# Kernel tuning notes

Hardware: AMD Instinct MI355X
Metric: run time of the kernel (lower is better)

The kernel has to match this reference:

```python
import jax, jax.numpy as jnp
import numpy as np

B, N, D, H, DK, DV, E = 32, 512, 128, 8, 16, 16, 128
MLP_H = 16


def _uniform(key, shape, fan):
    s = 1.0 / np.sqrt(fan)
    return jax.random.uniform(key, shape, jnp.float32, -s, s)


def setup_inputs() -> dict:
    key = jax.random.key(0)
    ks = jax.random.split(key, 13)
    q = jax.random.normal(ks[0], (B, N, D), jnp.float32)
    mask = jax.random.randint(ks[1], (B, N, N), 0, 2) > 0  # True = attention not allowed
    edge_matrix = jax.random.normal(ks[2], (B, N, N), jnp.float32)
    # per-head projection weights (init: uniform(-1/sqrt(last_dim), ...))
    W_query = _uniform(ks[3], (H, D, DK), DK)
    W_key = _uniform(ks[4], (H, D, DK), DK)
    W_val = _uniform(ks[5], (H, D, DV), DV)
    W_out = _uniform(ks[6], (H, DV, E), E)
    # edge MLP: 1 -> 16 -> 16 -> n_heads, ReLU between layers
    mlp_W1 = _uniform(ks[7], (1, MLP_H), 1)
    mlp_b1 = _uniform(ks[8], (MLP_H,), 1)
    mlp_W2 = _uniform(ks[9], (MLP_H, MLP_H), MLP_H)
    mlp_b2 = _uniform(ks[10], (MLP_H,), MLP_H)
    mlp_W3 = _uniform(ks[11], (MLP_H, H), MLP_H)
    mlp_b3 = _uniform(ks[12], (H,), MLP_H)
    return dict(q=q, mask=mask, edge_matrix=edge_matrix,
                W_query=W_query, W_key=W_key, W_val=W_val, W_out=W_out,
                mlp_W1=mlp_W1, mlp_b1=mlp_b1, mlp_W2=mlp_W2, mlp_b2=mlp_b2,
                mlp_W3=mlp_W3, mlp_b3=mlp_b3)


def reference(q, mask, edge_matrix, W_query, W_key, W_val, W_out,
              mlp_W1, mlp_b1, mlp_W2, mlp_b2, mlp_W3, mlp_b3):
    dk = W_query.shape[-1]
    norm = 1.0 / np.sqrt(dk)
    # per-head projections: [H,B,N,dk]
    Q = jnp.einsum('bni,hid->hbnd', q, W_query)
    K = jnp.einsum('bni,hid->hbnd', q, W_key)
    V = jnp.einsum('bni,hid->hbnd', q, W_val)
    # scaled QK^T: [H,B,N,N]
    comp = norm * jnp.einsum('hbqd,hbkd->hbqk', Q, K)
    # edge-bias MLP on each scalar edge weight: [B,N,N,1] -> [B,N,N,H]
    e = edge_matrix[..., None]
    h1 = jax.nn.relu(e @ mlp_W1 + mlp_b1)
    h2 = jax.nn.relu(h1 @ mlp_W2 + mlp_b2)
    bias = h2 @ mlp_W3 + mlp_b3
    comp = comp + jnp.transpose(bias, (3, 0, 1, 2))
    # masked softmax (mask True = disallowed)
    m = mask[None]  # broadcast over heads
    comp = jnp.where(m, -jnp.inf, comp)
    attn = jax.nn.softmax(comp, axis=-1)
    attn = jnp.where(m, 0.0, attn)
    heads = jnp.einsum('hbqk,hbkd->hbqd', attn, V)  # [H,B,N,dv]
    out = jnp.einsum('hbqd,hde->bqe', heads, W_out)  # [B,N,E]
    return out
```

## Files before the change

kernel.cpp:

```cpp
#include <hip/hip_runtime.h>
#include <hip/hip_bf16.h>
#include <float.h>

#define Bc 32
#define Nc 512
#define Dc 128
#define Hc 8
#define DKc 16
#define Ec 128
#define LOG2E 1.44269504088896340736f
#define SCLAMP 80.0f

typedef __attribute__((ext_vector_type(4))) short s16x4;
typedef __attribute__((ext_vector_type(8))) short s16x8;
typedef __attribute__((ext_vector_type(4))) float f32x4;

union BFU { __hip_bfloat16 b; short s; };
static __device__ inline short f2bf(float f) { BFU u; u.b = __float2bfloat16(f); return u.s; }
static __device__ inline s16x4 pack4(float a, float b, float c, float d) {
  s16x4 r; r[0] = f2bf(a); r[1] = f2bf(b); r[2] = f2bf(c); r[3] = f2bf(d); return r;
}

#if __has_builtin(__builtin_amdgcn_exp2f)
#define EXP2F(x) __builtin_amdgcn_exp2f(x)
#else
#define EXP2F(x) exp2f(x)
#endif

static __device__ inline f32x4 mfma16(s16x4 a, s16x4 b, f32x4 c) {
#if __has_builtin(__builtin_amdgcn_mfma_f32_16x16x16bf16_1k)
  return __builtin_amdgcn_mfma_f32_16x16x16bf16_1k(a, b, c, 0, 0, 0);
#else
  int lane = threadIdx.x & 63;
  int g = lane >> 4, base = lane & 15;
  int src0 = (base + 32 * g) & 63;
  int src1 = (base + 32 * g + 16) & 63;
  int ax = ((int*)&a)[0], ay = ((int*)&a)[1];
  int bx = ((int*)&b)[0], by = ((int*)&b)[1];
  int A0 = __shfl(ax, src0), A1 = __shfl(ay, src0);
  int A2 = __shfl(ax, src1), A3 = __shfl(ay, src1);
  int B0 = __shfl(bx, src0), B1 = __shfl(by, src0);
  int B2 = __shfl(bx, src1), B3 = __shfl(by, src1);
  if (g >= 2) { A0 = A1 = A2 = A3 = 0; B0 = B1 = B2 = B3 = 0; }
  s16x8 A8, B8;
  ((int*)&A8)[0] = A0; ((int*)&A8)[1] = A1; ((int*)&A8)[2] = A2; ((int*)&A8)[3] = A3;
  ((int*)&B8)[0] = B0; ((int*)&B8)[1] = B1; ((int*)&B8)[2] = B2; ((int*)&B8)[3] = B3;
  return __builtin_amdgcn_mfma_f32_16x16x32_bf16(A8, B8, c, 0, 0, 0);
#endif
}

__global__ __launch_bounds__(256) void prep_all(
    const float* __restrict__ Wq, const float* __restrict__ Wk, const float* __restrict__ Wv,
    const float* __restrict__ Wo,
    const unsigned char* __restrict__ m, int* __restrict__ flag,
    const float* __restrict__ mW1, const float* __restrict__ mb1,
    const float* __restrict__ mW2, const float* __restrict__ mb2,
    const float* __restrict__ mW3, const float* __restrict__ mb3,
    short* __restrict__ Wt, short* __restrict__ Wob, int* __restrict__ tabI)
{
  int blk = blockIdx.x;
  int t = threadIdx.x;

  if (blk == 256) {
    __shared__ int red[4];
    int any = 0;
    for (int u = t; u < 16384; u += 256)
      if ((u & 3) != 0 && m[u] != 0) any = 1;
    unsigned long long bal = __ballot(any != 0);
    if ((t & 63) == 0) red[t >> 6] = (bal != 0ULL) ? 1 : 0;
    __syncthreads();
    if (t == 0) *flag = red[0] | red[1] | red[2] | red[3];
    return;
  }

  if (blk >= 257) {
    __shared__ float wl[440];
    for (int u = t; u < 440; u += 256) {
      float v;
      if (u < 16) v = mW1[u];
      else if (u < 32)  v = mb1[u - 16];
      else if (u < 288) v = mW2[u - 32];
      else if (u < 304) v = mb2[u - 288];
      else if (u < 432) v = mW3[u - 304];
      else v = mb3[u - 432];
      wl[u] = v;
    }
    __syncthreads();
    int c = (blk - 257) * 256 + t;
    float mm = fmaf((float)c, 0.015625f, -7.9921875f);

    float pre[16];
    #pragma unroll
    for (int u = 0; u < 16; ++u) pre[u] = fmaf(mm, wl[u], wl[16 + u]);
    float a2[16], v2[16];
    #pragma unroll
    for (int v = 0; v < 16; ++v) { a2[v] = 0.f; v2[v] = wl[288 + v]; }
    #pragma unroll
    for (int u = 0; u < 16; ++u) {
      bool act = pre[u] > 0.f;
      float w1 = act ? wl[u] : 0.f;
      float pp = act ? pre[u] : 0.f;
      #pragma unroll
      for (int v = 0; v < 16; ++v) {
        float w2 = wl[32 + u * 16 + v];
        a2[v] = fmaf(w1, w2, a2[v]);
        v2[v] = fmaf(pp, w2, v2[v]);
      }
    }
    float ah[8], fh[8];
    #pragma unroll
    for (int h = 0; h < 8; ++h) { ah[h] = 0.f; fh[h] = wl[432 + h]; }
    #pragma unroll
    for (int v = 0; v < 16; ++v) {
      bool act = v2[v] > 0.f;
      float av = act ? a2[v] : 0.f;
      float vv = act ? v2[v] : 0.f;
      #pragma unroll
      for (int h = 0; h < 8; ++h) {
        float w3 = wl[304 + v * 8 + h];
        ah[h] = fmaf(av, w3, ah[h]);
        fh[h] = fmaf(vv, w3, fh[h]);
      }
    }
    #pragma unroll
    for (int h = 0; h < 8; ++h) {
      int ab = (int)(unsigned short)(f2bf(ah[h] * LOG2E));
      int fb = ((int)f2bf(fh[h] * LOG2E)) << 16;
      tabI[h * 1024 + c] = fb | ab;
    }
    return;
  }

  int o = blk * 256 + t;
  if (o < 49152) {
    int mat = o >> 14, r = o & 16383;
    int hk = r >> 7, d = r & 127;
    const float* src = (mat == 0) ? Wq : ((mat == 1) ? Wk : Wv);
    Wt[o] = f2bf(src[(hk >> 4) * 2048 + d * 16 + (hk & 15)]);
  } else {
    int o2 = o - 49152;
    int et = o2 >> 11, s = (o2 >> 8) & 7, lane = (o2 >> 2) & 63, i = o2 & 3;
    Wob[o2] = f2bf(Wo[(s * 16 + (lane >> 4) * 4 + i) * 128 + et * 16 + (lane & 15)]);
  }
}

__global__ __launch_bounds__(256, 4) void qkv4(
    const float* __restrict__ q, const short* __restrict__ Wt,
    short* __restrict__ Qb, short* __restrict__ Kb, short* __restrict__ Vt)
{
  __shared__ short qs[16][136];
  int blk = blockIdx.x;
  int b = blk >> 5;
  int rt = (blk & 31) << 4;
  int t = threadIdx.x;
  int wid = t >> 6, lane = t & 63;
  int lq = lane & 15, lg = lane >> 4;

  #pragma unroll
  for (int it = 0; it < 2; ++it) {
    int u = t + it * 256;
    int row = u >> 5, c4 = (u & 31) << 2;
    float4 v = *(const float4*)&q[((((b << 9) + rt + row) << 7)) + c4];
    *(s16x4*)&qs[row][c4] = pack4(v.x, v.y, v.z, v.w);
  }
  __syncthreads();

  s16x4 af[8];
  #pragma unroll
  for (int ks = 0; ks < 8; ++ks)
    af[ks] = *(const s16x4*)&qs[lq][ks * 16 + lg * 4];

  #pragma unroll 1
  for (int pj = 0; pj < 3; ++pj) {
    const short* Wm = Wt + pj * 16384;
    #pragma unroll
    for (int c2 = 0; c2 < 2; ++c2) {
      int ct = wid * 2 + c2;
      f32x4 acc = (f32x4)0.f;
      #pragma unroll
      for (int ks = 0; ks < 8; ++ks) {
        s16x4 bf = *(const s16x4*)&Wm[(ct * 16 + lq) * 128 + ks * 16 + lg * 4];
        acc = mfma16(af[ks], bf, acc);
      }
      if (pj == 0) {
        s16x4 pk = pack4(acc[0] * (0.25f * LOG2E), acc[1] * (0.25f * LOG2E),
                         acc[2] * (0.25f * LOG2E), acc[3] * (0.25f * LOG2E));
        #pragma unroll
        for (int r = 0; r < 4; ++r)
          Qb[(ct << 18) + (b << 13) + ((rt + lg * 4 + r) << 4) + lq] = pk[r];
      } else if (pj == 1) {
        s16x4 pk = pack4(acc[0], acc[1], acc[2], acc[3]);
        #pragma unroll
        for (int r = 0; r < 4; ++r)
          Kb[(ct << 18) + (b << 13) + ((rt + lg * 4 + r) << 4) + lq] = pk[r];
      } else {
        s16x4 pk = pack4(acc[0], acc[1], acc[2], acc[3]);
        *(s16x4*)&Vt[(ct << 18) + (((b << 4) + lq) << 9) + rt + lg * 4] = pk;
      }
    }
  }
}

__global__ __launch_bounds__(512, 4) void attn11(
    const float* __restrict__ edge, const unsigned char* __restrict__ maskB,
    const int* __restrict__ flag,
    const short* __restrict__ Qb, const short* __restrict__ Kb, const short* __restrict__ Vt,
    const short* __restrict__ Wob,
    const int* __restrict__ tabI,
    float* __restrict__ out)
{
  __shared__ __align__(16) char smem[36864];

  int t = threadIdx.x;
  int wid = t >> 6, lane = t & 63;
  int lq = lane & 15, lg = lane >> 4;
  int b = blockIdx.x >> 5;
  int qt = (blockIdx.x & 31) << 4;
  int mflag = *flag;

  int* tabL = (int*)smem;
  s16x4* obfL = (s16x4*)smem;
  float* psL = (float*)(smem + 32768);

  for (int u = t; u < 2048; u += 512)
    ((int4*)smem)[u] = ((const int4*)tabI)[u];

  const short* Kl = Kb + (b << 13) + (lq << 4) + (lg << 2);
  const short* Vl = Vt + (((b << 4) + lq) << 9) + (lg << 2);
  const short* Ql = Qb + (b << 13) + ((qt + lq) << 4) + (lg << 2);
  unsigned mbase = (((b << 9) + qt + lq) << 9) + (lg << 2);

  s16x4 qf[8];
  #pragma unroll
  for (int h = 0; h < 8; ++h) qf[h] = *(const s16x4*)(Ql + (h << 18));

  f32x4 oacc[8];
  float psum[8];
  #pragma unroll
  for (int h = 0; h < 8; ++h) { oacc[h] = (f32x4)0.f; psum[h] = 0.f; }

  int jb = wid << 4;
  float4 ev = *(const float4*)&edge[mbase + jb];
  int4 mkv;
  if (mflag) {
    uchar4 u = *(const uchar4*)&maskB[mbase + jb];
    mkv.x = u.x; mkv.y = u.y; mkv.z = u.z; mkv.w = u.w;
  } else {
    mkv = *(const int4*)&((const int*)maskB)[mbase + jb];
  }

  __syncthreads();

#define DOHEAD(h) { \
    int c0 = tabL[((h) << 10) + ix0], c1 = tabL[((h) << 10) + ix1]; \
    int c2 = tabL[((h) << 10) + ix2], c3 = tabL[((h) << 10) + ix3]; \
    s16x4 kf = *(const s16x4*)(Kl + ((h) << 18) + (jb << 4)); \
    f32x4 sc; \
    sc[0] = fmaf(__int_as_float(c0 << 16), em0, __int_as_float(c0 & 0xffff0000)); \
    sc[1] = fmaf(__int_as_float(c1 << 16), em1, __int_as_float(c1 & 0xffff0000)); \
    sc[2] = fmaf(__int_as_float(c2 << 16), em2, __int_as_float(c2 & 0xffff0000)); \
    sc[3] = fmaf(__int_as_float(c3 << 16), em3, __int_as_float(c3 & 0xffff0000)); \
    sc = mfma16(kf, qf[h], sc); \
    s16x4 vf = *(const s16x4*)(Vl + ((h) << 18) + jb); \
    float p0 = mkv.x ? 0.f : EXP2F(fminf(sc[0], SCLAMP)); \
    float p1 = mkv.y ? 0.f : EXP2F(fminf(sc[1], SCLAMP)); \
    float p2 = mkv.z ? 0.f : EXP2F(fminf(sc[2], SCLAMP)); \
    float p3 = mkv.w ? 0.f : EXP2F(fminf(sc[3], SCLAMP)); \
    psum[h] += (p0 + p1) + (p2 + p3); \
    s16x4 pf = pack4(p0, p1, p2, p3); \
    oacc[h] = mfma16(vf, pf, oacc[h]); }

  #pragma unroll 1
  for (int cc = 0; cc < 4; ++cc) {
    jb = ((cc << 3) | wid) << 4;

    float fx0 = fminf(fmaxf(fmaf(ev.x, 64.f, 512.f), 0.f), 1023.f);
    float fx1 = fminf(fmaxf(fmaf(ev.y, 64.f, 512.f), 0.f), 1023.f);
    float fx2 = fminf(fmaxf(fmaf(ev.z, 64.f, 512.f), 0.f), 1023.f);
    float fx3 = fminf(fmaxf(fmaf(ev.w, 64.f, 512.f), 0.f), 1023.f);
    int ix0 = (int)fx0, ix1 = (int)fx1, ix2 = (int)fx2, ix3 = (int)fx3;
    float em0 = ev.x - fmaf((float)ix0, 0.015625f, -7.9921875f);
    float em1 = ev.y - fmaf((float)ix1, 0.015625f, -7.9921875f);
    float em2 = ev.z - fmaf((float)ix2, 0.015625f, -7.9921875f);
    float em3 = ev.w - fmaf((float)ix3, 0.015625f, -7.9921875f);

    float4 evn; int4 mkn;
    if (cc < 3) {
      int jbn = (((cc + 1) << 3) | wid) << 4;
      evn = *(const float4*)&edge[mbase + jbn];
      if (mflag) {
        uchar4 u = *(const uchar4*)&maskB[mbase + jbn];
        mkn.x = u.x; mkn.y = u.y; mkn.z = u.z; mkn.w = u.w;
      } else {
        mkn = *(const int4*)&((const int*)maskB)[mbase + jbn];
      }
    } else { evn = ev; mkn = mkv; }

    DOHEAD(0) DOHEAD(1) DOHEAD(2) DOHEAD(3)
    DOHEAD(4) DOHEAD(5) DOHEAD(6) DOHEAD(7)

    ev = evn; mkv = mkn;
  }
#undef DOHEAD

  #pragma unroll
  for (int h = 0; h < 8; ++h) {
    float s = psum[h];
    s += __shfl_xor(s, 16);
    s += __shfl_xor(s, 32);
    psum[h] = s;
  }
  if (lg == 0) {
    #pragma unroll
    for (int h = 0; h < 8; ++h) psL[(wid << 7) + (h << 4) + lq] = psum[h];
  }
  __syncthreads();

  #pragma unroll
  for (int h = 0; h < 8; ++h) {
    float tot = 0.f;
    #pragma unroll
    for (int w2 = 0; w2 < 8; ++w2) tot += psL[(w2 << 7) + (h << 4) + lq];
    float inv = (tot > 0.f) ? 1.f / tot : 0.f;
    obfL[((wid << 3) + h << 6) + lane] =
        pack4(oacc[h][0] * inv, oacc[h][1] * inv, oacc[h][2] * inv, oacc[h][3] * inv);
  }
  __syncthreads();

  {
    f32x4 d2a = (f32x4)0.f;
    #pragma unroll
    for (int s = 0; s < 8; ++s) {
      f32x4 fa = (f32x4)0.f;
      #pragma unroll
      for (int w2 = 0; w2 < 8; ++w2) {
        union { s16x4 v; int i[2]; } bb;
        bb.v = obfL[((w2 << 3) + s << 6) + lane];
        fa[0] += __int_as_float(bb.i[0] << 16);
        fa[1] += __int_as_float(bb.i[0] & 0xffff0000);
        fa[2] += __int_as_float(bb.i[1] << 16);
        fa[3] += __int_as_float(bb.i[1] & 0xffff0000);
      }
      s16x4 ob = pack4(fa[0], fa[1], fa[2], fa[3]);
      s16x4 wo = *(const s16x4*)&Wob[(((wid << 3) + s) << 8) + (lane << 2)];
      d2a = mfma16(wo, ob, d2a);
    }
    *(float4*)&out[((((b << 9) + qt + lq) << 7)) + (wid << 4) + (lg << 2)] =
        *(float4*)&d2a;
  }
}

extern "C" void kernel_launch(void* const* d_in, const int* in_sizes, int n_in,
                              void* d_out, int out_size, void* d_ws, size_t ws_size,
                              hipStream_t stream)
{
  const float* q    = (const float*)d_in[0];
  const unsigned char* mask = (const unsigned char*)d_in[1];
  const float* edge = (const float*)d_in[2];
  const float* Wq   = (const float*)d_in[3];
  const float* Wk   = (const float*)d_in[4];
  const float* Wv   = (const float*)d_in[5];
  const float* Wo   = (const float*)d_in[6];
  const float* mW1  = (const float*)d_in[7];
  const float* mb1  = (const float*)d_in[8];
  const float* mW2  = (const float*)d_in[9];
  const float* mb2  = (const float*)d_in[10];
  const float* mW3  = (const float*)d_in[11];
  const float* mb3  = (const float*)d_in[12];
  float* out = (float*)d_out;

  size_t per = (size_t)Hc * Bc * Nc * DKc;
  short* Wt  = (short*)d_ws;
  short* Wob = Wt + 49152;
  short* Qb  = Wob + 16384;
  short* Kb  = Qb + per;
  short* Vt  = Kb + per;
  int* tabI  = (int*)(Vt + per);
  int* flag  = tabI + 8192;

  prep_all<<<dim3(261), dim3(256), 0, stream>>>(Wq, Wk, Wv, Wo, mask, flag,
      mW1, mb1, mW2, mb2, mW3, mb3, Wt, Wob, tabI);
  qkv4<<<dim3(Bc * 32), dim3(256), 0, stream>>>(q, Wt, Qb, Kb, Vt);
  attn11<<<dim3(Bc * 32), dim3(512), 0, stream>>>(edge, mask, flag, Qb, Kb, Vt, Wob,
      tabI, out);
}
```

Before: 123.7 us.

## Assign one head per wave in attention kernel, removing cross-wave reduction

Each wave now processes a single head over all keys instead of all heads over a 1/8 key slice. This drops the LDS-based cross-wave reduction of softmax sums and output accumulators, shrinks per-thread state from eight accumulators to one, and lets each wave read its own head's slice of the edge-bias table. In exchange, every wave re-reads the full edge and mask rows for its queries, relying on cache to absorb the eightfold redundant loads.

New measurement: 146.9 us. 1.19x slower.

```diff
diff --git a/kernel.cpp b/kernel.cpp
--- a/kernel.cpp
+++ b/kernel.cpp
@@ -201,7 +201,7 @@
   }
 }
 
-__global__ __launch_bounds__(512, 4) void attn11(
+__global__ __launch_bounds__(512, 4) void attn12(
     const float* __restrict__ edge, const unsigned char* __restrict__ maskB,
     const int* __restrict__ flag,
     const short* __restrict__ Qb, const short* __restrict__ Kb, const short* __restrict__ Vt,
@@ -209,7 +209,7 @@
     const int* __restrict__ tabI,
     float* __restrict__ out)
 {
-  __shared__ __align__(16) char smem[36864];
+  __shared__ __align__(16) char smem[32768];
 
   int t = threadIdx.x;
   int wid = t >> 6, lane = t & 63;
@@ -218,61 +218,34 @@
   int qt = (blockIdx.x & 31) << 4;
   int mflag = *flag;
 
-  int* tabL = (int*)smem;
-  s16x4* obfL = (s16x4*)smem;
-  float* psL = (float*)(smem + 32768);
+  int* tabH = (int*)smem + (wid << 10);
 
   for (int u = t; u < 2048; u += 512)
     ((int4*)smem)[u] = ((const int4*)tabI)[u];
 
-  const short* Kl = Kb + (b << 13) + (lq << 4) + (lg << 2);
-  const short* Vl = Vt + (((b << 4) + lq) << 9) + (lg << 2);
-  const short* Ql = Qb + (b << 13) + ((qt + lq) << 4) + (lg << 2);
+  const short* Kl = Kb + (wid << 18) + (b << 13) + (lq << 4) + (lg << 2);
+  const short* Vl = Vt + (wid << 18) + (((b << 4) + lq) << 9) + (lg << 2);
+  const short* Ql = Qb + (wid << 18) + (b << 13) + ((qt + lq) << 4) + (lg << 2);
   unsigned mbase = (((b << 9) + qt + lq) << 9) + (lg << 2);
 
-  s16x4 qf[8];
-  #pragma unroll
-  for (int h = 0; h < 8; ++h) qf[h] = *(const s16x4*)(Ql + (h << 18));
-
-  f32x4 oacc[8];
-  float psum[8];
-  #pragma unroll
-  for (int h = 0; h < 8; ++h) { oacc[h] = (f32x4)0.f; psum[h] = 0.f; }
-
-  int jb = wid << 4;
-  float4 ev = *(const float4*)&edge[mbase + jb];
+  s16x4 qf = *(const s16x4*)Ql;
+  f32x4 oacc = (f32x4)0.f;
+  float psum = 0.f;
+
+  float4 ev = *(const float4*)&edge[mbase];
   int4 mkv;
   if (mflag) {
-    uchar4 u = *(const uchar4*)&maskB[mbase + jb];
+    uchar4 u = *(const uchar4*)&maskB[mbase];
     mkv.x = u.x; mkv.y = u.y; mkv.z = u.z; mkv.w = u.w;
   } else {
-    mkv = *(const int4*)&((const int*)maskB)[mbase + jb];
+    mkv = *(const int4*)&((const int*)maskB)[mbase];
   }
 
   __syncthreads();
 
-#define DOHEAD(h) { \
-    int c0 = tabL[((h) << 10) + ix0], c1 = tabL[((h) << 10) + ix1]; \
-    int c2 = tabL[((h) << 10) + ix2], c3 = tabL[((h) << 10) + ix3]; \
-    s16x4 kf = *(const s16x4*)(Kl + ((h) << 18) + (jb << 4)); \
-    f32x4 sc; \
-    sc[0] = fmaf(__int_as_float(c0 << 16), em0, __int_as_float(c0 & 0xffff0000)); \
-    sc[1] = fmaf(__int_as_float(c1 << 16), em1, __int_as_float(c1 & 0xffff0000)); \
-    sc[2] = fmaf(__int_as_float(c2 << 16), em2, __int_as_float(c2 & 0xffff0000)); \
-    sc[3] = fmaf(__int_as_float(c3 << 16), em3, __int_as_float(c3 & 0xffff0000)); \
-    sc = mfma16(kf, qf[h], sc); \
-    s16x4 vf = *(const s16x4*)(Vl + ((h) << 18) + jb); \
-    float p0 = mkv.x ? 0.f : EXP2F(fminf(sc[0], SCLAMP)); \
-    float p1 = mkv.y ? 0.f : EXP2F(fminf(sc[1], SCLAMP)); \
-    float p2 = mkv.z ? 0.f : EXP2F(fminf(sc[2], SCLAMP)); \
-    float p3 = mkv.w ? 0.f : EXP2F(fminf(sc[3], SCLAMP)); \
-    psum[h] += (p0 + p1) + (p2 + p3); \
-    s16x4 pf = pack4(p0, p1, p2, p3); \
-    oacc[h] = mfma16(vf, pf, oacc[h]); }
-
-  #pragma unroll 1
-  for (int cc = 0; cc < 4; ++cc) {
-    jb = ((cc << 3) | wid) << 4;
+  #pragma unroll 2
+  for (int cc = 0; cc < 32; ++cc) {
+    int jb = cc << 4;
 
     float fx0 = fminf(fmaxf(fmaf(ev.x, 64.f, 512.f), 0.f), 1023.f);
     float fx1 = fminf(fmaxf(fmaf(ev.y, 64.f, 512.f), 0.f), 1023.f);
@@ -284,9 +257,13 @@
     float em2 = ev.z - fmaf((float)ix2, 0.015625f, -7.9921875f);
     float em3 = ev.w - fmaf((float)ix3, 0.015625f, -7.9921875f);
 
+    int c0 = tabH[ix0], c1 = tabH[ix1], c2 = tabH[ix2], c3 = tabH[ix3];
+    s16x4 kf = *(const s16x4*)(Kl + (jb << 4));
+    s16x4 vf = *(const s16x4*)(Vl + jb);
+
     float4 evn; int4 mkn;
-    if (cc < 3) {
-      int jbn = (((cc + 1) << 3) | wid) << 4;
+    if (cc < 31) {
+      int jbn = (cc + 1) << 4;
       evn = *(const float4*)&edge[mbase + jbn];
       if (mflag) {
         uchar4 u = *(const uchar4*)&maskB[mbase + jbn];
@@ -296,53 +273,38 @@
       }
     } else { evn = ev; mkn = mkv; }
 
-    DOHEAD(0) DOHEAD(1) DOHEAD(2) DOHEAD(3)
-    DOHEAD(4) DOHEAD(5) DOHEAD(6) DOHEAD(7)
+    f32x4 sc;
+    sc[0] = fmaf(__int_as_float(c0 << 16), em0, __int_as_float(c0 & 0xffff0000));
+    sc[1] = fmaf(__int_as_float(c1 << 16), em1, __int_as_float(c1 & 0xffff0000));
+    sc[2] = fmaf(__int_as_float(c2 << 16), em2, __int_as_float(c2 & 0xffff0000));
+    sc[3] = fmaf(__int_as_float(c3 << 16), em3, __int_as_float(c3 & 0xffff0000));
+    sc = mfma16(kf, qf, sc);
+    float p0 = mkv.x ? 0.f : EXP2F(fminf(sc[0], SCLAMP));
+    float p1 = mkv.y ? 0.f : EXP2F(fminf(sc[1], SCLAMP));
+    float p2 = mkv.z ? 0.f : EXP2F(fminf(sc[2], SCLAMP));
+    float p3 = mkv.w ? 0.f : EXP2F(fminf(sc[3], SCLAMP));
+    psum += (p0 + p1) + (p2 + p3);
+    s16x4 pf = pack4(p0, p1, p2, p3);
+    oacc = mfma16(vf, pf, oacc);
 
     ev = evn; mkv = mkn;
   }
-#undef DOHEAD
-
-  #pragma unroll
-  for (int h = 0; h < 8; ++h) {
-    float s = psum[h];
-    s += __shfl_xor(s, 16);
-    s += __shfl_xor(s, 32);
-    psum[h] = s;
-  }
-  if (lg == 0) {
-    #pragma unroll
-    for (int h = 0; h < 8; ++h) psL[(wid << 7) + (h << 4) + lq] = psum[h];
-  }
-  __syncthreads();
-
-  #pragma unroll
-  for (int h = 0; h < 8; ++h) {
-    float tot = 0.f;
-    #pragma unroll
-    for (int w2 = 0; w2 < 8; ++w2) tot += psL[(w2 << 7) + (h << 4) + lq];
-    float inv = (tot > 0.f) ? 1.f / tot : 0.f;
-    obfL[((wid << 3) + h << 6) + lane] =
-        pack4(oacc[h][0] * inv, oacc[h][1] * inv, oacc[h][2] * inv, oacc[h][3] * inv);
-  }
+
+  float s = psum;
+  s += __shfl_xor(s, 16);
+  s += __shfl_xor(s, 32);
+  float inv = (s > 0.f) ? 1.f / s : 0.f;
+
+  *(s16x4*)(smem + (wid << 12) + lane * 8) =
+      pack4(oacc[0] * inv, oacc[1] * inv, oacc[2] * inv, oacc[3] * inv);
   __syncthreads();
 
   {
     f32x4 d2a = (f32x4)0.f;
     #pragma unroll
-    for (int s = 0; s < 8; ++s) {
-      f32x4 fa = (f32x4)0.f;
-      #pragma unroll
-      for (int w2 = 0; w2 < 8; ++w2) {
-        union { s16x4 v; int i[2]; } bb;
-        bb.v = obfL[((w2 << 3) + s << 6) + lane];
-        fa[0] += __int_as_float(bb.i[0] << 16);
-        fa[1] += __int_as_float(bb.i[0] & 0xffff0000);
-        fa[2] += __int_as_float(bb.i[1] << 16);
-        fa[3] += __int_as_float(bb.i[1] & 0xffff0000);
-      }
-      s16x4 ob = pack4(fa[0], fa[1], fa[2], fa[3]);
-      s16x4 wo = *(const s16x4*)&Wob[(((wid << 3) + s) << 8) + (lane << 2)];
+    for (int s8 = 0; s8 < 8; ++s8) {
+      s16x4 ob = *(const s16x4*)(smem + (s8 << 12) + lane * 8);
+      s16x4 wo = *(const s16x4*)&Wob[(((wid << 3) + s8) << 8) + (lane << 2)];
       d2a = mfma16(wo, ob, d2a);
     }
     *(float4*)&out[((((b << 9) + qt + lq) << 7)) + (wid << 4) + (lg << 2)] =
@@ -381,6 +343,6 @@
   prep_all<<<dim3(261), dim3(256), 0, stream>>>(Wq, Wk, Wv, Wo, mask, flag,
       mW1, mb1, mW2, mb2, mW3, mb3, Wt, Wob, tabI);
   qkv4<<<dim3(Bc * 32), dim3(256), 0, stream>>>(q, Wt, Qb, Kb, Vt);
-  attn11<<<dim3(Bc * 32), dim3(512), 0, stream>>>(edge, mask, flag, Qb, Kb, Vt, Wob,
+  attn12<<<dim3(Bc * 32), dim3(512), 0, stream>>>(edge, mask, flag, Qb, Kb, Vt, Wob,
       tabI, out);
 }
```

## Restructure attention loop head-outer with all edge/mask chunks preloaded up front

Applied to the files above, without the earlier changes.

The attention kernel now issues all four edge and mask chunk loads before staging the bias table into shared memory, so global latency overlaps the table copy. The loop changes from chunk-outer/head-inner with software prefetch to a fully unrolled head-outer loop that handles four key chunks per head. Table indices and residuals are precomputed once as byte offsets. This exposes more independent loads and MFMAs per head, but raises register pressure (16 indices, 16 residuals, 4 mask vectors) under the 512-thread launch bound, which may cause spills.

New measurement: 171.7 us. 1.39x slower.

```diff
diff --git a/kernel.cpp b/kernel.cpp
--- a/kernel.cpp
+++ b/kernel.cpp
@@ -201,7 +201,7 @@
   }
 }
 
-__global__ __launch_bounds__(512, 4) void attn11(
+__global__ __launch_bounds__(512, 4) void attn15(
     const float* __restrict__ edge, const unsigned char* __restrict__ maskB,
     const int* __restrict__ flag,
     const short* __restrict__ Qb, const short* __restrict__ Kb, const short* __restrict__ Vt,
@@ -218,18 +218,40 @@
   int qt = (blockIdx.x & 31) << 4;
   int mflag = *flag;
 
-  int* tabL = (int*)smem;
   s16x4* obfL = (s16x4*)smem;
   float* psL = (float*)(smem + 32768);
-
-  for (int u = t; u < 2048; u += 512)
-    ((int4*)smem)[u] = ((const int4*)tabI)[u];
 
   const short* Kl = Kb + (b << 13) + (lq << 4) + (lg << 2);
   const short* Vl = Vt + (((b << 4) + lq) << 9) + (lg << 2);
   const short* Ql = Qb + (b << 13) + ((qt + lq) << 4) + (lg << 2);
   unsigned mbase = (((b << 9) + qt + lq) << 9) + (lg << 2);
 
+  int jb0 = wid << 4, jb1 = (wid + 8) << 4, jb2 = (wid + 16) << 4, jb3 = (wid + 24) << 4;
+  float4 ev0 = *(const float4*)&edge[mbase + jb0];
+  float4 ev1 = *(const float4*)&edge[mbase + jb1];
+  float4 ev2 = *(const float4*)&edge[mbase + jb2];
+  float4 ev3 = *(const float4*)&edge[mbase + jb3];
+  int4 mk0, mk1, mk2, mk3;
+  if (mflag) {
+    uchar4 u0 = *(const uchar4*)&maskB[mbase + jb0];
+    uchar4 u1 = *(const uchar4*)&maskB[mbase + jb1];
+    uchar4 u2 = *(const uchar4*)&maskB[mbase + jb2];
+    uchar4 u3 = *(const uchar4*)&maskB[mbase + jb3];
+    mk0.x = u0.x; mk0.y = u0.y; mk0.z = u0.z; mk0.w = u0.w;
+    mk1.x = u1.x; mk1.y = u1.y; mk1.z = u1.z; mk1.w = u1.w;
+    mk2.x = u2.x; mk2.y = u2.y; mk2.z = u2.z; mk2.w = u2.w;
+    mk3.x = u3.x; mk3.y = u3.y; mk3.z = u3.z; mk3.w = u3.w;
+  } else {
+    const int* mi = (const int*)maskB;
+    mk0 = *(const int4*)&mi[mbase + jb0];
+    mk1 = *(const int4*)&mi[mbase + jb1];
+    mk2 = *(const int4*)&mi[mbase + jb2];
+    mk3 = *(const int4*)&mi[mbase + jb3];
+  }
+
+  for (int u = t; u < 2048; u += 512)
+    ((int4*)smem)[u] = ((const int4*)tabI)[u];
+
   s16x4 qf[8];
   #pragma unroll
   for (int h = 0; h < 8; ++h) qf[h] = *(const s16x4*)(Ql + (h << 18));
@@ -239,69 +261,82 @@
   #pragma unroll
   for (int h = 0; h < 8; ++h) { oacc[h] = (f32x4)0.f; psum[h] = 0.f; }
 
-  int jb = wid << 4;
-  float4 ev = *(const float4*)&edge[mbase + jb];
-  int4 mkv;
-  if (mflag) {
-    uchar4 u = *(const uchar4*)&maskB[mbase + jb];
-    mkv.x = u.x; mkv.y = u.y; mkv.z = u.z; mkv.w = u.w;
-  } else {
-    mkv = *(const int4*)&((const int*)maskB)[mbase + jb];
+  unsigned ab[16];
+  float em[16];
+  {
+    const float* evp[4] = { (const float*)&ev0, (const float*)&ev1,
+                            (const float*)&ev2, (const float*)&ev3 };
+    #pragma unroll
+    for (int s = 0; s < 4; ++s)
+      #pragma unroll
+      for (int r = 0; r < 4; ++r) {
+        float e = evp[s][r];
+        float fx = fminf(fmaxf(fmaf(e, 64.f, 512.f), 0.f), 1023.f);
+        int ix = (int)fx;
+        ab[s * 4 + r] = (unsigned)(ix << 2);
+        em[s * 4 + r] = e - fmaf((float)ix, 0.015625f, -7.9921875f);
+      }
   }
 
   __syncthreads();
 
-#define DOHEAD(h) { \
-    int c0 = tabL[((h) << 10) + ix0], c1 = tabL[((h) << 10) + ix1]; \
-    int c2 = tabL[((h) << 10) + ix2], c3 = tabL[((h) << 10) + ix3]; \
-    s16x4 kf = *(const s16x4*)(Kl + ((h) << 18) + (jb << 4)); \
-    f32x4 sc; \
-    sc[0] = fmaf(__int_as_float(c0 << 16), em0, __int_as_float(c0 & 0xffff0000)); \
-    sc[1] = fmaf(__int_as_float(c1 << 16), em1, __int_as_float(c1 & 0xffff0000)); \
-    sc[2] = fmaf(__int_as_float(c2 << 16), em2, __int_as_float(c2 & 0xffff0000)); \
-    sc[3] = fmaf(__int_as_float(c3 << 16), em3, __int_as_float(c3 & 0xffff0000)); \
-    sc = mfma16(kf, qf[h], sc); \
-    s16x4 vf = *(const s16x4*)(Vl + ((h) << 18) + jb); \
-    float p0 = mkv.x ? 0.f : EXP2F(fminf(sc[0], SCLAMP)); \
-    float p1 = mkv.y ? 0.f : EXP2F(fminf(sc[1], SCLAMP)); \
-    float p2 = mkv.z ? 0.f : EXP2F(fminf(sc[2], SCLAMP)); \
-    float p3 = mkv.w ? 0.f : EXP2F(fminf(sc[3], SCLAMP)); \
-    psum[h] += (p0 + p1) + (p2 + p3); \
-    s16x4 pf = pack4(p0, p1, p2, p3); \
-    oacc[h] = mfma16(vf, pf, oacc[h]); }
-
-  #pragma unroll 1
-  for (int cc = 0; cc < 4; ++cc) {
-    jb = ((cc << 3) | wid) << 4;
-
-    float fx0 = fminf(fmaxf(fmaf(ev.x, 64.f, 512.f), 0.f), 1023.f);
-    float fx1 = fminf(fmaxf(fmaf(ev.y, 64.f, 512.f), 0.f), 1023.f);
-    float fx2 = fminf(fmaxf(fmaf(ev.z, 64.f, 512.f), 0.f), 1023.f);
-    float fx3 = fminf(fmaxf(fmaf(ev.w, 64.f, 512.f), 0.f), 1023.f);
-    int ix0 = (int)fx0, ix1 = (int)fx1, ix2 = (int)fx2, ix3 = (int)fx3;
-    float em0 = ev.x - fmaf((float)ix0, 0.015625f, -7.9921875f);
-    float em1 = ev.y - fmaf((float)ix1, 0.015625f, -7.9921875f);
-    float em2 = ev.z - fmaf((float)ix2, 0.015625f, -7.9921875f);
-    float em3 = ev.w - fmaf((float)ix3, 0.015625f, -7.9921875f);
-
-    float4 evn; int4 mkn;
-    if (cc < 3) {
-      int jbn = (((cc + 1) << 3) | wid) << 4;
-      evn = *(const float4*)&edge[mbase + jbn];
-      if (mflag) {
-        uchar4 u = *(const uchar4*)&maskB[mbase + jbn];
-        mkn.x = u.x; mkn.y = u.y; mkn.z = u.z; mkn.w = u.w;
-      } else {
-        mkn = *(const int4*)&((const int*)maskB)[mbase + jbn];
-      }
-    } else { evn = ev; mkn = mkv; }
-
-    DOHEAD(0) DOHEAD(1) DOHEAD(2) DOHEAD(3)
-    DOHEAD(4) DOHEAD(5) DOHEAD(6) DOHEAD(7)
-
-    ev = evn; mkv = mkn;
-  }
-#undef DOHEAD
+  #pragma unroll
+  for (int h = 0; h < 8; ++h) {
+    const char* tb = smem + (h << 12);
+    int c[16];
+    #pragma unroll
+    for (int u = 0; u < 16; ++u) c[u] = *(const int*)(tb + ab[u]);
+    s16x4 kf0 = *(const s16x4*)(Kl + (h << 18) + (jb0 << 4));
+    s16x4 kf1 = *(const s16x4*)(Kl + (h << 18) + (jb1 << 4));
+    s16x4 kf2 = *(const s16x4*)(Kl + (h << 18) + (jb2 << 4));
+    s16x4 kf3 = *(const s16x4*)(Kl + (h << 18) + (jb3 << 4));
+    s16x4 vf0 = *(const s16x4*)(Vl + (h << 18) + jb0);
+    s16x4 vf1 = *(const s16x4*)(Vl + (h << 18) + jb1);
+    s16x4 vf2 = *(const s16x4*)(Vl + (h << 18) + jb2);
+    s16x4 vf3 = *(const s16x4*)(Vl + (h << 18) + jb3);
+
+    f32x4 s0, s1, s2, s3;
+    #pragma unroll
+    for (int r = 0; r < 4; ++r) {
+      s0[r] = fmaf(__int_as_float(c[r] << 16),      em[r],      __int_as_float(c[r] & 0xffff0000));
+      s1[r] = fmaf(__int_as_float(c[4 + r] << 16),  em[4 + r],  __int_as_float(c[4 + r] & 0xffff0000));
+      s2[r] = fmaf(__int_as_float(c[8 + r] << 16),  em[8 + r],  __int_as_float(c[8 + r] & 0xffff0000));
+      s3[r] = fmaf(__int_as_float(c[12 + r] << 16), em[12 + r], __int_as_float(c[12 + r] & 0xffff0000));
+    }
+    s0 = mfma16(kf0, qf[h], s0);
+    s1 = mfma16(kf1, qf[h], s1);
+    s2 = mfma16(kf2, qf[h], s2);
+    s3 = mfma16(kf3, qf[h], s3);
+
+    float p00 = mk0.x ? 0.f : EXP2F(fminf(s0[0], SCLAMP));
+    float p01 = mk0.y ? 0.f : EXP2F(fminf(s0[1], SCLAMP));
+    float p02 = mk0.z ? 0.f : EXP2F(fminf(s0[2], SCLAMP));
+    float p03 = mk0.w ? 0.f : EXP2F(fminf(s0[3], SCLAMP));
+    float p10 = mk1.x ? 0.f : EXP2F(fminf(s1[0], SCLAMP));
+    float p11 = mk1.y ? 0.f : EXP2F(fminf(s1[1], SCLAMP));
+    float p12 = mk1.z ? 0.f : EXP2F(fminf(s1[2], SCLAMP));
+    float p13 = mk1.w ? 0.f : EXP2F(fminf(s1[3], SCLAMP));
+    float p20 = mk2.x ? 0.f : EXP2F(fminf(s2[0], SCLAMP));
+    float p21 = mk2.y ? 0.f : EXP2F(fminf(s2[1], SCLAMP));
+    float p22 = mk2.z ? 0.f : EXP2F(fminf(s2[2], SCLAMP));
+    float p23 = mk2.w ? 0.f : EXP2F(fminf(s2[3], SCLAMP));
+    float p30 = mk3.x ? 0.f : EXP2F(fminf(s3[0], SCLAMP));
+    float p31 = mk3.y ? 0.f : EXP2F(fminf(s3[1], SCLAMP));
+    float p32 = mk3.z ? 0.f : EXP2F(fminf(s3[2], SCLAMP));
+    float p33 = mk3.w ? 0.f : EXP2F(fminf(s3[3], SCLAMP));
+
+    psum[h] += (((p00 + p01) + (p02 + p03)) + ((p10 + p11) + (p12 + p13)))
+             + (((p20 + p21) + (p22 + p23)) + ((p30 + p31) + (p32 + p33)));
+
+    s16x4 pf0 = pack4(p00, p01, p02, p03);
+    s16x4 pf1 = pack4(p10, p11, p12, p13);
+    s16x4 pf2 = pack4(p20, p21, p22, p23);
+    s16x4 pf3 = pack4(p30, p31, p32, p33);
+    oacc[h] = mfma16(vf0, pf0, oacc[h]);
+    oacc[h] = mfma16(vf1, pf1, oacc[h]);
+    oacc[h] = mfma16(vf2, pf2, oacc[h]);
+    oacc[h] = mfma16(vf3, pf3, oacc[h]);
+  }
 
   #pragma unroll
   for (int h = 0; h < 8; ++h) {
@@ -381,6 +416,6 @@
   prep_all<<<dim3(261), dim3(256), 0, stream>>>(Wq, Wk, Wv, Wo, mask, flag,
       mW1, mb1, mW2, mb2, mW3, mb3, Wt, Wob, tabI);
   qkv4<<<dim3(Bc * 32), dim3(256), 0, stream>>>(q, Wt, Qb, Kb, Vt);
-  attn11<<<dim3(Bc * 32), dim3(512), 0, stream>>>(edge, mask, flag, Qb, Kb, Vt, Wob,
+  attn15<<<dim3(Bc * 32), dim3(512), 0, stream>>>(edge, mask, flag, Qb, Kb, Vt, Wob,
       tabI, out);
 }
```
